# Performance work log

Measured on AMD Instinct MI355X. Metric: run time of the kernel, lower is better.

## Reference

```python
import jax, jax.numpy as jnp
import numpy as np

MARGIN = 0.2
EPS = 1e-5
NEG_SENTINEL = -1e9


def _cos_sim(a, b):
    a = a / jnp.linalg.norm(a, axis=-1, keepdims=True)
    b = b / jnp.linalg.norm(b, axis=-1, keepdims=True)
    return a @ b.T  # [B, B]


def _row_losses(sm, labels):
    # sm: [B, B] similarity matrix; one loop body of the original, vectorized over rows i.
    diag = jnp.diagonal(sm)                      # pos_pair_ (scalar per row)
    pos_valid = diag < (1.0 - EPS)               # pos_pair_[pos_pair_ < 1-eps]
    neg_mask = labels[None, :] != labels[:, None]
    # neg_pair_[neg_pair_ + margin > min(pos_pair_)] ; min of a scalar is itself
    hard = neg_mask & ((sm + MARGIN) > diag[:, None])
    has_neg = jnp.any(hard, axis=1)
    neg_max = jnp.max(jnp.where(hard, sm, NEG_SENTINEL), axis=1)  # max(neg_pair)
    valid = pos_valid & has_neg
    pos_loss = jnp.maximum(0.2 * diag * diag - 0.7 * diag + 0.5, 0.0)
    neg_loss = jnp.maximum(0.9 * neg_max * neg_max - 0.4 * neg_max + 0.03, 0.0)
    return jnp.sum(jnp.where(valid, pos_loss + neg_loss, 0.0))


def setup_inputs() -> dict:
    key = jax.random.key(0)
    k1, k2 = jax.random.split(key)
    B, D = 8192, 256
    audio_embeds = jax.random.normal(k1, (B, D), dtype=jnp.float32)
    text_embeds = jax.random.normal(k2, (B, D), dtype=jnp.float32)
    labels = jnp.arange(B, dtype=jnp.int64)
    return {"audio_embeds": audio_embeds, "text_embeds": text_embeds, "labels": labels}


def reference(audio_embeds, text_embeds, labels):
    scores = _cos_sim(audio_embeds, text_embeds)  # [B, B]
    B = scores.shape[0]
    total = _row_losses(scores, labels) + _row_losses(scores.T, labels)
    return total / B
```

## Files before the change

kernel.cpp:

```cpp
#include <hip/hip_runtime.h>
#include <stdint.h>

#define BM 128
#define BN 128
#define KD 256

typedef __attribute__((ext_vector_type(4))) float f32x4;
typedef __attribute__((ext_vector_type(4))) int   i32x4;
typedef __attribute__((ext_vector_type(8))) int   i32x8;

__global__ __launch_bounds__(256) void norm_kernel(
    const float* __restrict__ a, const float* __restrict__ b,
    unsigned int* __restrict__ an, unsigned int* __restrict__ bn,
    float* __restrict__ diag, float* __restrict__ out, int D) {
  if (blockIdx.x == 0 && threadIdx.x == 0) out[0] = 0.f;
  const int row = blockIdx.x * 4 + (threadIdx.x >> 6);
  const int l = threadIdx.x & 63;
  const float4 av = ((const float4*)(a + (size_t)row * D))[l];
  const float4 bv = ((const float4*)(b + (size_t)row * D))[l];
  float ssa = av.x*av.x + av.y*av.y + av.z*av.z + av.w*av.w;
  float ssb = bv.x*bv.x + bv.y*bv.y + bv.z*bv.z + bv.w*bv.w;
  float dot = av.x*bv.x + av.y*bv.y + av.z*bv.z + av.w*bv.w;
  for (int off = 1; off < 64; off <<= 1) {
    ssa += __shfl_xor(ssa, off, 64);
    ssb += __shfl_xor(ssb, off, 64);
    dot += __shfl_xor(dot, off, 64);
  }
  const float inva = 1.0f / sqrtf(ssa);
  const float invb = 1.0f / sqrtf(ssb);
  if (l == 0) diag[row] = dot * inva * invb;
  int pa = 0, pb = 0;
  pa = __builtin_amdgcn_cvt_pk_fp8_f32(av.x * inva, av.y * inva, pa, 0);
  pa = __builtin_amdgcn_cvt_pk_fp8_f32(av.z * inva, av.w * inva, pa, 1);
  pb = __builtin_amdgcn_cvt_pk_fp8_f32(bv.x * invb, bv.y * invb, pb, 0);
  pb = __builtin_amdgcn_cvt_pk_fp8_f32(bv.z * invb, bv.w * invb, pb, 1);
  an[(size_t)row * (D / 4) + l] = (unsigned int)pa;
  bn[(size_t)row * (D / 4) + l] = (unsigned int)pb;
}

__global__ __launch_bounds__(256, 2) void gemm_max_kernel(
    const unsigned char* __restrict__ an, const unsigned char* __restrict__ bn,
    const int* __restrict__ labels,
    float* __restrict__ row_part, float* __restrict__ col_part, int B) {
  __shared__ __align__(16) unsigned char sA[2][BM * 128];
  __shared__ __align__(16) unsigned char sB[2][BN * 128];
  __shared__ float lds_row[2][BM];
  __shared__ float lds_col[2][BN];

  const int tid  = threadIdx.x;
  const int lane = tid & 63;
  const int w    = tid >> 6;
  const int wm   = w >> 1, wn = w & 1;
  const int tj   = blockIdx.x & 63;
  const int ti   = blockIdx.x >> 6;

  const int sr  = lane >> 3;
  const int sc8 = lane & 7;
  const int ssw = (sc8 ^ sr) * 16;
  #pragma unroll
  for (int it = 0; it < 2; ++it) {
    #pragma unroll
    for (int c = 0; c < 4; ++c) {
      const int r0 = w * 32 + c * 8;
      const unsigned char* ga = an + (size_t)(ti * BM + r0 + sr) * KD + it * 128 + ssw;
      const unsigned char* gb = bn + (size_t)(tj * BN + r0 + sr) * KD + it * 128 + ssw;
      __builtin_amdgcn_global_load_lds(
          (const __attribute__((address_space(1))) void*)ga,
          (__attribute__((address_space(3))) void*)(&sA[it][r0 * 128] + lane * 16), 16, 0, 0);
      __builtin_amdgcn_global_load_lds(
          (const __attribute__((address_space(1))) void*)gb,
          (__attribute__((address_space(3))) void*)(&sB[it][r0 * 128] + lane * 16), 16, 0, 0);
    }
  }

  const int fr = lane & 15;
  const int hi = lane >> 4;
  const int p0 = ((2 * hi)     ^ (fr & 7)) * 16;
  const int p1 = ((2 * hi + 1) ^ (fr & 7)) * 16;

  int li[4][4], labc[4];
  #pragma unroll
  for (int mt = 0; mt < 4; ++mt)
    #pragma unroll
    for (int r = 0; r < 4; ++r)
      li[mt][r] = labels[ti * BM + wm * 64 + mt * 16 + hi * 4 + r];
  #pragma unroll
  for (int nt = 0; nt < 4; ++nt)
    labc[nt] = labels[tj * BN + wn * 64 + nt * 16 + fr];

  f32x4 acc[4][4];
  #pragma unroll
  for (int mt = 0; mt < 4; ++mt)
    #pragma unroll
    for (int nt = 0; nt < 4; ++nt)
      acc[mt][nt] = (f32x4){0.f, 0.f, 0.f, 0.f};

  __syncthreads();

  const int SC = 0x7F7F7F7F;
  #pragma unroll
  for (int it = 0; it < 2; ++it) {
    i32x8 af[4], bf[4];
    #pragma unroll
    for (int t = 0; t < 4; ++t) {
      const unsigned char* ra = &sA[it][(wm * 64 + t * 16 + fr) * 128];
      const unsigned char* rb = &sB[it][(wn * 64 + t * 16 + fr) * 128];
      i32x4 alo = *(const i32x4*)(ra + p0), ahi = *(const i32x4*)(ra + p1);
      i32x4 blo = *(const i32x4*)(rb + p0), bhi = *(const i32x4*)(rb + p1);
      af[t] = __builtin_shufflevector(alo, ahi, 0, 1, 2, 3, 4, 5, 6, 7);
      bf[t] = __builtin_shufflevector(blo, bhi, 0, 1, 2, 3, 4, 5, 6, 7);
    }
    #pragma unroll
    for (int mt = 0; mt < 4; ++mt)
      #pragma unroll
      for (int nt = 0; nt < 4; ++nt)
        acc[mt][nt] = __builtin_amdgcn_mfma_scale_f32_16x16x128_f8f6f4(
            af[mt], bf[nt], acc[mt][nt], 0, 0, 0, SC, 0, SC);
  }

  float cmax[4] = {-1e9f, -1e9f, -1e9f, -1e9f};
  #pragma unroll
  for (int mt = 0; mt < 4; ++mt)
    #pragma unroll
    for (int r = 0; r < 4; ++r) {
      const int l0 = li[mt][r];
      float rmax = -1e9f;
      #pragma unroll
      for (int nt = 0; nt < 4; ++nt) {
        const float vm = (l0 != labc[nt]) ? acc[mt][nt][r] : -1e9f;
        rmax = fmaxf(rmax, vm);
        cmax[nt] = fmaxf(cmax[nt], vm);
      }
      #pragma unroll
      for (int off = 1; off < 16; off <<= 1)
        rmax = fmaxf(rmax, __shfl_xor(rmax, off, 64));
      if (fr == 0) lds_row[wn][wm * 64 + mt * 16 + hi * 4 + r] = rmax;
    }
  #pragma unroll
  for (int nt = 0; nt < 4; ++nt) {
    float c = cmax[nt];
    c = fmaxf(c, __shfl_xor(c, 16, 64));
    c = fmaxf(c, __shfl_xor(c, 32, 64));
    if (hi == 0) lds_col[wm][wn * 64 + nt * 16 + fr] = c;
  }
  __syncthreads();
  if (tid < BM)
    row_part[(size_t)tj * B + ti * BM + tid] =
        fmaxf(lds_row[0][tid], lds_row[1][tid]);
  else if (tid < BM + BN) {
    const int t2 = tid - BM;
    col_part[(size_t)ti * B + tj * BN + t2] =
        fmaxf(lds_col[0][t2], lds_col[1][t2]);
  }
}

__global__ __launch_bounds__(256) void finalize_kernel(
    const float* __restrict__ row_part, const float* __restrict__ col_part,
    const float* __restrict__ diag, int B, int T, float* __restrict__ out) {
  const int v = blockIdx.x * 256 + threadIdx.x;
  const bool isrow = v < B;
  const int i = isrow ? v : v - B;
  const float* part = isrow ? row_part : col_part;
  float m = -1e9f;
  for (int t = 0; t < T; ++t) m = fmaxf(m, part[(size_t)t * B + i]);
  const float d = diag[i];
  float loss = 0.f;
  if ((d < 1.0f - 1e-5f) && (m + 0.2f > d)) {
    loss = fmaxf(0.2f * d * d - 0.7f * d + 0.5f, 0.f) +
           fmaxf(0.9f * m * m - 0.4f * m + 0.03f, 0.f);
  }
  for (int off = 1; off < 64; off <<= 1) loss += __shfl_xor(loss, off, 64);
  __shared__ float ssum[4];
  if ((threadIdx.x & 63) == 0) ssum[threadIdx.x >> 6] = loss;
  __syncthreads();
  if (threadIdx.x == 0)
    atomicAdd(out, (ssum[0] + ssum[1] + ssum[2] + ssum[3]) / (float)B);
}

extern "C" void kernel_launch(void* const* d_in, const int* in_sizes, int n_in,
                              void* d_out, int out_size, void* d_ws, size_t ws_size,
                              hipStream_t stream) {
  const float* a      = (const float*)d_in[0];
  const float* b      = (const float*)d_in[1];
  const int*   labels = (const int*)d_in[2];
  const int B = in_sizes[2];
  const int D = in_sizes[0] / B;
  const int T = B / BM;

  char* ws = (char*)d_ws;
  unsigned char* an = (unsigned char*)ws;
  unsigned char* bn = (unsigned char*)(ws + (size_t)B * D);
  float* diag     = (float*)(ws + (size_t)2 * B * D);
  float* row_part = diag + B;
  float* col_part = row_part + (size_t)T * B;

  norm_kernel<<<B / 4, 256, 0, stream>>>(a, b, (unsigned int*)an,
                                         (unsigned int*)bn, diag,
                                         (float*)d_out, D);

  gemm_max_kernel<<<(B / BM) * (B / BN), 256, 0, stream>>>(
      an, bn, labels, row_part, col_part, B);

  finalize_kernel<<<(2 * B) / 256, 256, 0, stream>>>(
      row_part, col_part, diag, B, T, (float*)d_out);
}
```

Baseline: 137.7 us.

## Halve LDS staging, raise occupancy, replace row shuffle reduction with LDS transpose

```diff
diff --git a/kernel.cpp b/kernel.cpp
--- a/kernel.cpp
+++ b/kernel.cpp
@@ -8,6 +8,10 @@
 typedef __attribute__((ext_vector_type(4))) float f32x4;
 typedef __attribute__((ext_vector_type(4))) int   i32x4;
 typedef __attribute__((ext_vector_type(8))) int   i32x8;
+
+__device__ __forceinline__ float fmax4(f32x4 v) {
+  return fmaxf(fmaxf(v[0], v[1]), fmaxf(v[2], v[3]));
+}
 
 __global__ __launch_bounds__(256) void norm_kernel(
     const float* __restrict__ a, const float* __restrict__ b,
@@ -38,13 +42,12 @@
   bn[(size_t)row * (D / 4) + l] = (unsigned int)pb;
 }
 
-__global__ __launch_bounds__(256, 2) void gemm_max_kernel(
+__global__ __launch_bounds__(256, 4) void gemm_max_kernel(
     const unsigned char* __restrict__ an, const unsigned char* __restrict__ bn,
     const int* __restrict__ labels,
     float* __restrict__ row_part, float* __restrict__ col_part, int B) {
-  __shared__ __align__(16) unsigned char sA[2][BM * 128];
-  __shared__ __align__(16) unsigned char sB[2][BN * 128];
-  __shared__ float lds_row[2][BM];
+  __shared__ __align__(16) unsigned char sA[BM * 128];
+  __shared__ __align__(16) unsigned char sB[BN * 128];
   __shared__ float lds_col[2][BN];
 
   const int tid  = threadIdx.x;
@@ -57,6 +60,21 @@
   const int sr  = lane >> 3;
   const int sc8 = lane & 7;
   const int ssw = (sc8 ^ sr) * 16;
+
+  const int fr = lane & 15;
+  const int hi = lane >> 4;
+  const int p0 = ((2 * hi)     ^ (fr & 7)) * 16;
+  const int p1 = ((2 * hi + 1) ^ (fr & 7)) * 16;
+
+  f32x4 acc[4][4];
+  #pragma unroll
+  for (int mt = 0; mt < 4; ++mt)
+    #pragma unroll
+    for (int nt = 0; nt < 4; ++nt)
+      acc[mt][nt] = (f32x4){0.f, 0.f, 0.f, 0.f};
+
+  const int SC = 0x7F7F7F7F;
+
   #pragma unroll
   for (int it = 0; it < 2; ++it) {
     #pragma unroll
@@ -66,88 +84,91 @@
       const unsigned char* gb = bn + (size_t)(tj * BN + r0 + sr) * KD + it * 128 + ssw;
       __builtin_amdgcn_global_load_lds(
           (const __attribute__((address_space(1))) void*)ga,
-          (__attribute__((address_space(3))) void*)(&sA[it][r0 * 128] + lane * 16), 16, 0, 0);
+          (__attribute__((address_space(3))) void*)(sA + r0 * 128 + lane * 16), 16, 0, 0);
       __builtin_amdgcn_global_load_lds(
           (const __attribute__((address_space(1))) void*)gb,
-          (__attribute__((address_space(3))) void*)(&sB[it][r0 * 128] + lane * 16), 16, 0, 0);
-    }
-  }
-
-  const int fr = lane & 15;
-  const int hi = lane >> 4;
-  const int p0 = ((2 * hi)     ^ (fr & 7)) * 16;
-  const int p1 = ((2 * hi + 1) ^ (fr & 7)) * 16;
-
-  int li[4][4], labc[4];
-  #pragma unroll
-  for (int mt = 0; mt < 4; ++mt)
-    #pragma unroll
-    for (int r = 0; r < 4; ++r)
-      li[mt][r] = labels[ti * BM + wm * 64 + mt * 16 + hi * 4 + r];
-  #pragma unroll
-  for (int nt = 0; nt < 4; ++nt)
-    labc[nt] = labels[tj * BN + wn * 64 + nt * 16 + fr];
-
-  f32x4 acc[4][4];
-  #pragma unroll
-  for (int mt = 0; mt < 4; ++mt)
-    #pragma unroll
-    for (int nt = 0; nt < 4; ++nt)
-      acc[mt][nt] = (f32x4){0.f, 0.f, 0.f, 0.f};
-
-  __syncthreads();
-
-  const int SC = 0x7F7F7F7F;
-  #pragma unroll
-  for (int it = 0; it < 2; ++it) {
-    i32x8 af[4], bf[4];
-    #pragma unroll
-    for (int t = 0; t < 4; ++t) {
-      const unsigned char* ra = &sA[it][(wm * 64 + t * 16 + fr) * 128];
-      const unsigned char* rb = &sB[it][(wn * 64 + t * 16 + fr) * 128];
+          (__attribute__((address_space(3))) void*)(sB + r0 * 128 + lane * 16), 16, 0, 0);
+    }
+    __syncthreads();
+
+    i32x8 bf[4];
+    #pragma unroll
+    for (int nt = 0; nt < 4; ++nt) {
+      const unsigned char* rb = sB + (wn * 64 + nt * 16 + fr) * 128;
+      i32x4 blo = *(const i32x4*)(rb + p0), bhi = *(const i32x4*)(rb + p1);
+      bf[nt] = __builtin_shufflevector(blo, bhi, 0, 1, 2, 3, 4, 5, 6, 7);
+    }
+    #pragma unroll
+    for (int mt = 0; mt < 4; ++mt) {
+      const unsigned char* ra = sA + (wm * 64 + mt * 16 + fr) * 128;
       i32x4 alo = *(const i32x4*)(ra + p0), ahi = *(const i32x4*)(ra + p1);
-      i32x4 blo = *(const i32x4*)(rb + p0), bhi = *(const i32x4*)(rb + p1);
-      af[t] = __builtin_shufflevector(alo, ahi, 0, 1, 2, 3, 4, 5, 6, 7);
-      bf[t] = __builtin_shufflevector(blo, bhi, 0, 1, 2, 3, 4, 5, 6, 7);
-    }
-    #pragma unroll
-    for (int mt = 0; mt < 4; ++mt)
+      i32x8 af = __builtin_shufflevector(alo, ahi, 0, 1, 2, 3, 4, 5, 6, 7);
       #pragma unroll
       for (int nt = 0; nt < 4; ++nt)
         acc[mt][nt] = __builtin_amdgcn_mfma_scale_f32_16x16x128_f8f6f4(
-            af[mt], bf[nt], acc[mt][nt], 0, 0, 0, SC, 0, SC);
-  }
-
-  float cmax[4] = {-1e9f, -1e9f, -1e9f, -1e9f};
+            af, bf[nt], acc[mt][nt], 0, 0, 0, SC, 0, SC);
+    }
+    __syncthreads();
+  }
+
+  int li[4][4], labc[4];
+  #pragma unroll
+  for (int mt = 0; mt < 4; ++mt)
+    #pragma unroll
+    for (int r = 0; r < 4; ++r)
+      li[mt][r] = labels[ti * BM + wm * 64 + mt * 16 + hi * 4 + r];
+  #pragma unroll
+  for (int nt = 0; nt < 4; ++nt)
+    labc[nt] = labels[tj * BN + wn * 64 + nt * 16 + fr];
+
+  float rp[4][4];
+  float cp[4] = {-1e9f, -1e9f, -1e9f, -1e9f};
   #pragma unroll
   for (int mt = 0; mt < 4; ++mt)
     #pragma unroll
     for (int r = 0; r < 4; ++r) {
       const int l0 = li[mt][r];
-      float rmax = -1e9f;
+      float rm = -1e9f;
       #pragma unroll
       for (int nt = 0; nt < 4; ++nt) {
         const float vm = (l0 != labc[nt]) ? acc[mt][nt][r] : -1e9f;
-        rmax = fmaxf(rmax, vm);
-        cmax[nt] = fmaxf(cmax[nt], vm);
+        rm = fmaxf(rm, vm);
+        cp[nt] = fmaxf(cp[nt], vm);
       }
-      #pragma unroll
-      for (int off = 1; off < 16; off <<= 1)
-        rmax = fmaxf(rmax, __shfl_xor(rmax, off, 64));
-      if (fr == 0) lds_row[wn][wm * 64 + mt * 16 + hi * 4 + r] = rmax;
-    }
+      rp[mt][r] = rm;
+    }
+
+  float* red = (float*)sA;
+  const int s = wn * 16 + fr;
+  #pragma unroll
+  for (int mt = 0; mt < 4; ++mt)
+    #pragma unroll
+    for (int r = 0; r < 4; ++r) {
+      const int i = wm * 64 + mt * 16 + hi * 4 + r;
+      red[i * 32 + (((s >> 2) ^ (i & 7)) << 2) + (s & 3)] = rp[mt][r];
+    }
+
   #pragma unroll
   for (int nt = 0; nt < 4; ++nt) {
-    float c = cmax[nt];
+    float c = cp[nt];
     c = fmaxf(c, __shfl_xor(c, 16, 64));
     c = fmaxf(c, __shfl_xor(c, 32, 64));
     if (hi == 0) lds_col[wm][wn * 64 + nt * 16 + fr] = c;
   }
   __syncthreads();
-  if (tid < BM)
-    row_part[(size_t)tj * B + ti * BM + tid] =
-        fmaxf(lds_row[0][tid], lds_row[1][tid]);
-  else if (tid < BM + BN) {
+
+  if (tid < BM) {
+    const int key = tid & 7;
+    const f32x4* rr = (const f32x4*)(red + tid * 32);
+    f32x4 m4 = rr[0 ^ key];
+    #pragma unroll
+    for (int k = 1; k < 8; ++k) {
+      f32x4 v = rr[k ^ key];
+      m4[0] = fmaxf(m4[0], v[0]); m4[1] = fmaxf(m4[1], v[1]);
+      m4[2] = fmaxf(m4[2], v[2]); m4[3] = fmaxf(m4[3], v[3]);
+    }
+    row_part[(size_t)tj * B + ti * BM + tid] = fmax4(m4);
+  } else if (tid < BM + BN) {
     const int t2 = tid - BM;
     col_part[(size_t)ti * B + tj * BN + t2] =
         fmaxf(lds_col[0][t2], lds_col[1][t2]);
```

New measurement: 121.1 us. 1.14x faster.
